# Kernel tuning notes

Hardware: AMD Instinct MI355X
Metric: run time of the kernel (lower is better)

## Reference

```python
import jax, jax.numpy as jnp
import numpy as np

NEG_INF = -9e15  # matches the torch -9000000000000000.0 mask value
LRELU_SLOPE = 0.01  # torch nn.LeakyReLU default


def setup_inputs() -> dict:
    key = jax.random.key(0)
    k1, k2, k3, k4 = jax.random.split(key, 4)
    N, F_in, F_out = 8192, 256, 128
    x = jax.random.normal(k1, (N, F_in), dtype=jnp.float32)
    adj = jax.random.randint(k2, (N, N), 0, 2, dtype=jnp.int32)
    # xavier_uniform with gain=1.414
    limW = 1.414 * np.sqrt(6.0 / (F_in + F_out))
    W = jax.random.uniform(k3, (F_in, F_out), minval=-limW, maxval=limW, dtype=jnp.float32)
    lima = 1.414 * np.sqrt(6.0 / (2 * F_out + 1))
    a = jax.random.uniform(k4, (2 * F_out, 1), minval=-lima, maxval=lima, dtype=jnp.float32)
    return {"x": x, "adj": adj, "W": W, "a": a}


def reference(x, adj, W, a):
    # h: [N, F_out]
    h = x @ W
    F_out = h.shape[1]
    a1 = a[:F_out, 0]   # attention vector for source node i
    a2 = a[F_out:, 0]   # attention vector for target node j
    # e[i, j] = leaky_relu(h_i . a1 + h_j . a2) -- equivalent to the repeat/cat
    # construction without materializing the [N, N, 2F] tensor.
    e = (h @ a1)[:, None] + (h @ a2)[None, :]  # [N, N]
    e = jnp.where(e > 0, e, LRELU_SLOPE * e)
    scores = jnp.where(adj > 0, e, NEG_INF)
    attention = jax.nn.softmax(scores, axis=1)  # dropout omitted (eval mode)
    h_prime = attention @ h  # [N, F_out]
    return jax.nn.elu(h_prime)
```

## Files before the change

### kernel.cpp

```cpp
#include <hip/hip_runtime.h>
#include <hip/hip_bf16.h>
#include <stdint.h>


#define N_NODES 8192
#define F_INF   256
#define F_OUT   128
#define LRELU   0.01f

typedef __bf16 bf16x8 __attribute__((ext_vector_type(8)));
typedef float  f32x4  __attribute__((ext_vector_type(4)));
using bf16 = __hip_bfloat16;

__device__ __forceinline__ float b2f(bf16 v) { return __bfloat162float(v); }
__device__ __forceinline__ bf16  f2b(float v) { return __float2bfloat16(v); }

__global__ __launch_bounds__(256) void k_xw(const float* __restrict__ x,
                                            const float* __restrict__ W,
                                            const float* __restrict__ a,
                                            bf16* __restrict__ hT,
                                            float* __restrict__ s1,
                                            float* __restrict__ s2) {
    __shared__ __align__(16) bf16 WTh[F_OUT][F_INF + 8];
    __shared__ __align__(16) bf16 WTl[F_OUT][F_INF + 8];
    __shared__ __align__(16) bf16 XSh[32][72];
    __shared__ __align__(16) bf16 XSl[32][72];
    __shared__ float a1s[F_OUT], a2s[F_OUT], s1L[32], s2L[32];
    const int tid  = threadIdx.x;
    const int lane = tid & 63, wave = tid >> 6;
    const int i0   = blockIdx.x * 32;
    if (tid < F_OUT) { a1s[tid] = a[tid]; a2s[tid] = a[tid + F_OUT]; }
    if (tid < 32)    { s1L[tid] = 0.f; s2L[tid] = 0.f; }
    for (int idx = tid; idx < (F_INF * F_OUT) / 8; idx += 256) {
        int k  = idx >> 4;
        int n0 = (idx & 15) * 8;
        const float* src = W + (size_t)k * F_OUT + n0;
        float4 va = *(const float4*)(src);
        float4 vb = *(const float4*)(src + 4);
        float v[8] = {va.x, va.y, va.z, va.w, vb.x, vb.y, vb.z, vb.w};
#pragma unroll
        for (int c = 0; c < 8; ++c) {
            bf16 hi = f2b(v[c]);
            WTh[n0 + c][k] = hi;
            WTl[n0 + c][k] = f2b(v[c] - b2f(hi));
        }
    }
    __syncthreads();
    f32x4 acc[4];
#pragma unroll
    for (int t = 0; t < 4; ++t) acc[t] = {0.f, 0.f, 0.f, 0.f};
    const int m = lane & 15, quad = lane >> 4;
    const int rt = wave & 1, cH = wave >> 1;
    for (int kc = 0; kc < F_INF / 64; ++kc) {
        const int k0 = kc * 64;
        {
            int part = tid & 7;
            int r    = tid >> 3;
            const float* src = x + (size_t)(i0 + r) * F_INF + k0 + part * 8;
            float4 va = *(const float4*)(src);
            float4 vb = *(const float4*)(src + 4);
            float v[8] = {va.x, va.y, va.z, va.w, vb.x, vb.y, vb.z, vb.w};
            __align__(16) bf16 th[8];
            __align__(16) bf16 tl[8];
#pragma unroll
            for (int c = 0; c < 8; ++c) {
                bf16 hi = f2b(v[c]);
                th[c] = hi;
                tl[c] = f2b(v[c] - b2f(hi));
            }
            *(uint4*)(&XSh[r][part * 8]) = *(const uint4*)th;
            *(uint4*)(&XSl[r][part * 8]) = *(const uint4*)tl;
        }
        __syncthreads();
#pragma unroll
        for (int ks = 0; ks < 2; ++ks) {
            bf16x8 ah = *(const bf16x8*)(&XSh[rt * 16 + m][ks * 32 + quad * 8]);
            bf16x8 al = *(const bf16x8*)(&XSl[rt * 16 + m][ks * 32 + quad * 8]);
#pragma unroll
            for (int c = 0; c < 4; ++c) {
                const int ct = cH * 4 + c;
                bf16x8 bh = *(const bf16x8*)(&WTh[ct * 16 + m][k0 + ks * 32 + quad * 8]);
                bf16x8 bl = *(const bf16x8*)(&WTl[ct * 16 + m][k0 + ks * 32 + quad * 8]);
                acc[c] = __builtin_amdgcn_mfma_f32_16x16x32_bf16(al, bh, acc[c], 0, 0, 0);
                acc[c] = __builtin_amdgcn_mfma_f32_16x16x32_bf16(ah, bl, acc[c], 0, 0, 0);
                acc[c] = __builtin_amdgcn_mfma_f32_16x16x32_bf16(ah, bh, acc[c], 0, 0, 0);
            }
        }
        __syncthreads();
    }
    float p1[4] = {0.f, 0.f, 0.f, 0.f}, p2[4] = {0.f, 0.f, 0.f, 0.f};
#pragma unroll
    for (int c = 0; c < 4; ++c) {
        const int f = (cH * 4 + c) * 16 + m;
        const float w1 = a1s[f], w2 = a2s[f];
#pragma unroll
        for (int r = 0; r < 4; ++r) { p1[r] += acc[c][r] * w1; p2[r] += acc[c][r] * w2; }
    }
#pragma unroll
    for (int r = 0; r < 4; ++r) {
        const int row = rt * 16 + quad * 4 + r;
        atomicAdd(&s1L[row], p1[r]);
        atomicAdd(&s2L[row], p2[r]);
    }
#pragma unroll
    for (int c = 0; c < 4; ++c) {
        const int f = (cH * 4 + c) * 16 + m;
#pragma unroll
        for (int r = 0; r < 4; ++r) {
            const int i = i0 + rt * 16 + quad * 4 + r;
            hT[(size_t)f * N_NODES + i] = f2b(acc[c][r]);
        }
    }
    __syncthreads();
    if (tid < 32) { s1[i0 + tid] = s1L[tid]; s2[i0 + tid] = s2L[tid]; }
}

__global__ __launch_bounds__(256) void k_max(const float* __restrict__ s2,
                                             float* __restrict__ mg) {
    __shared__ float red[256];
    int tid = threadIdx.x;
    float m = -1e30f;
    for (int j = tid; j < N_NODES; j += 256) m = fmaxf(m, s2[j]);
    red[tid] = m;
    __syncthreads();
    for (int s = 128; s > 0; s >>= 1) {
        if (tid < s) red[tid] = fmaxf(red[tid], red[tid + s]);
        __syncthreads();
    }
    if (tid == 0) mg[0] = red[0];
}

__global__ __launch_bounds__(256) void k_attn(const int* __restrict__ adj,
                                              const float* __restrict__ s1g,
                                              const float* __restrict__ s2g,
                                              const float* __restrict__ mg,
                                              const bf16* __restrict__ hT,
                                              float* __restrict__ Of,
                                              float* __restrict__ lp) {
    __shared__ __align__(16) bf16 HS[F_OUT][72];
    __shared__ __align__(16) bf16 PS[32][72];
    __shared__ float s1s[32], mis[32], lsum[32];
    const int tid  = threadIdx.x;
    const int lane = tid & 63, wave = tid >> 6;
    const int i0    = blockIdx.x * 32;
    const int jq    = blockIdx.y;
    const int jbase = jq * (N_NODES / 4);
    if (tid < 32) {
        float s1v = s1g[i0 + tid];
        float t   = s1v + mg[0];
        s1s[tid]  = s1v;
        mis[tid]  = t > 0.f ? t : LRELU * t;
        lsum[tid] = 0.f;
    }
    __syncthreads();
    const int jpart = tid & 15;
    const int rA    = tid >> 4;
    float lacc0 = 0.f, lacc1 = 0.f;
    const int m = lane & 15, quad = lane >> 4;
    const int cg = wave;
    f32x4 acc[2][2];
#pragma unroll
    for (int rt = 0; rt < 2; ++rt)
#pragma unroll
        for (int c = 0; c < 2; ++c) acc[rt][c] = {0.f, 0.f, 0.f, 0.f};

    for (int jc = 0; jc < (N_NODES / 4) / 64; ++jc) {
        const int j0 = jbase + jc * 64;
        {
            int part = tid & 7, fr = tid >> 3;
#pragma unroll
            for (int p = 0; p < 4; ++p) {
                int f   = fr + p * 32;
                uint4 v = *(const uint4*)(hT + (size_t)f * N_NODES + j0 + part * 8);
                *(uint4*)(&HS[f][part * 8]) = v;
            }
        }
        {
            float4 s2v = *(const float4*)(s2g + j0 + jpart * 4);
#pragma unroll
            for (int p = 0; p < 2; ++p) {
                int r = rA + p * 16;
                const int4 av = *(const int4*)(adj + (size_t)(i0 + r) * N_NODES + j0 + jpart * 4);
                const float s1v = s1s[r], miv = mis[r];
                float t;
                t = s1v + s2v.x; t = t > 0.f ? t : LRELU * t;
                bf16 b0 = f2b((av.x > 0) ? __expf(t - miv) : 0.f);
                t = s1v + s2v.y; t = t > 0.f ? t : LRELU * t;
                bf16 b1 = f2b((av.y > 0) ? __expf(t - miv) : 0.f);
                t = s1v + s2v.z; t = t > 0.f ? t : LRELU * t;
                bf16 b2 = f2b((av.z > 0) ? __expf(t - miv) : 0.f);
                t = s1v + s2v.w; t = t > 0.f ? t : LRELU * t;
                bf16 b3 = f2b((av.w > 0) ? __expf(t - miv) : 0.f);
                float wsum = (b2f(b0) + b2f(b1)) + (b2f(b2) + b2f(b3));
                if (p == 0) lacc0 += wsum; else lacc1 += wsum;
                PS[r][jpart * 4 + 0] = b0;
                PS[r][jpart * 4 + 1] = b1;
                PS[r][jpart * 4 + 2] = b2;
                PS[r][jpart * 4 + 3] = b3;
            }
        }
        __syncthreads();
#pragma unroll
        for (int ks = 0; ks < 2; ++ks) {
#pragma unroll
            for (int rt = 0; rt < 2; ++rt) {
                bf16x8 af = *(const bf16x8*)(&PS[rt * 16 + m][ks * 32 + quad * 8]);
#pragma unroll
                for (int c = 0; c < 2; ++c) {
                    bf16x8 bfr = *(const bf16x8*)(&HS[(cg * 2 + c) * 16 + m][ks * 32 + quad * 8]);
                    acc[rt][c] = __builtin_amdgcn_mfma_f32_16x16x32_bf16(af, bfr, acc[rt][c], 0, 0, 0);
                }
            }
        }
        __syncthreads();
    }
    atomicAdd(&lsum[rA], lacc0);
    atomicAdd(&lsum[rA + 16], lacc1);
    __syncthreads();
    if (tid < 32) lp[(size_t)jq * N_NODES + i0 + tid] = lsum[tid];
#pragma unroll
    for (int rt = 0; rt < 2; ++rt) {
#pragma unroll
        for (int c = 0; c < 2; ++c) {
            const int f = (cg * 2 + c) * 16 + m;
#pragma unroll
            for (int r = 0; r < 4; ++r) {
                const int i = i0 + rt * 16 + quad * 4 + r;
                Of[((size_t)jq * N_NODES + i) * F_OUT + f] = acc[rt][c][r];
            }
        }
    }
}

__global__ __launch_bounds__(256) void k_comb(const float* __restrict__ Of,
                                              const float* __restrict__ lp,
                                              float* __restrict__ out) {
    size_t gid = (size_t)blockIdx.x * 256 + threadIdx.x;
    int i = (int)(gid >> 7);
    float s = 0.f, l = 0.f;
#pragma unroll
    for (int q = 0; q < 4; ++q) {
        s += Of[(size_t)q * (N_NODES * (size_t)F_OUT) + gid];
        l += lp[q * N_NODES + i];
    }
    float o = s / l;
    out[gid] = o > 0.f ? o : __expf(o) - 1.f;
}

extern "C" void kernel_launch(void* const* d_in, const int* in_sizes, int n_in,
                              void* d_out, int out_size, void* d_ws, size_t ws_size,
                              hipStream_t stream) {
    (void)out_size; (void)ws_size;
    const float* x   = nullptr;
    const int*   adj = nullptr;
    const float* W   = nullptr;
    const float* a   = nullptr;
    for (int ii = 0; ii < n_in; ++ii) {
        int sz = in_sizes[ii];
        if      (sz == N_NODES * F_INF)  x   = (const float*)d_in[ii];
        else if (sz == F_INF * F_OUT)    W   = (const float*)d_in[ii];
        else if (sz == 2 * F_OUT)        a   = (const float*)d_in[ii];
        else                             adj = (const int*)d_in[ii];
    }
    float* out = (float*)d_out;

    char* ws = (char*)d_ws;
    bf16*  hT = (bf16*)ws;  ws += (size_t)F_OUT * N_NODES * 2;
    float* s1 = (float*)ws; ws += N_NODES * 4;
    float* s2 = (float*)ws; ws += N_NODES * 4;
    float* mg = (float*)ws; ws += 256;
    float* lp = (float*)ws; ws += 4 * N_NODES * 4;
    float* Of = (float*)ws;

    k_xw  <<<N_NODES / 32, 256, 0, stream>>>(x, W, a, hT, s1, s2);
    k_max <<<1, 256, 0, stream>>>(s2, mg);
    k_attn<<<dim3(N_NODES / 32, 4), 256, 0, stream>>>(adj, s1, s2, mg, hT, Of, lp);
    k_comb<<<(N_NODES * F_OUT) / 256, 256, 0, stream>>>(Of, lp, out);
}
```

Baseline: 441.1 us.

## Compute attention weights in registers as MFMA A-fragments and prefetch next tiles

```diff
diff --git a/kernel.cpp b/kernel.cpp
--- a/kernel.cpp
+++ b/kernel.cpp
@@ -130,105 +130,109 @@
     if (tid == 0) mg[0] = red[0];
 }
 
-__global__ __launch_bounds__(256) void k_attn(const int* __restrict__ adj,
-                                              const float* __restrict__ s1g,
-                                              const float* __restrict__ s2g,
-                                              const float* __restrict__ mg,
-                                              const bf16* __restrict__ hT,
-                                              float* __restrict__ Of,
-                                              float* __restrict__ lp) {
+__global__ __launch_bounds__(256, 4) void k_attn(const int* __restrict__ adj,
+                                                 const float* __restrict__ s1g,
+                                                 const float* __restrict__ s2g,
+                                                 const float* __restrict__ mg,
+                                                 const bf16* __restrict__ hT,
+                                                 float* __restrict__ Of,
+                                                 float* __restrict__ lp) {
     __shared__ __align__(16) bf16 HS[F_OUT][72];
-    __shared__ __align__(16) bf16 PS[32][72];
-    __shared__ float s1s[32], mis[32], lsum[32];
+    __shared__ float s2s[2048];
+    __shared__ float lsum[32];
     const int tid  = threadIdx.x;
     const int lane = tid & 63, wave = tid >> 6;
+    const int m = lane & 15, quad = lane >> 4;
+    const int rt = wave & 1, kh = wave >> 1;
     const int i0    = blockIdx.x * 32;
     const int jq    = blockIdx.y;
-    const int jbase = jq * (N_NODES / 4);
-    if (tid < 32) {
-        float s1v = s1g[i0 + tid];
-        float t   = s1v + mg[0];
-        s1s[tid]  = s1v;
-        mis[tid]  = t > 0.f ? t : LRELU * t;
-        lsum[tid] = 0.f;
-    }
-    __syncthreads();
-    const int jpart = tid & 15;
-    const int rA    = tid >> 4;
-    float lacc0 = 0.f, lacc1 = 0.f;
-    const int m = lane & 15, quad = lane >> 4;
-    const int cg = wave;
-    f32x4 acc[2][2];
-#pragma unroll
-    for (int rt = 0; rt < 2; ++rt)
-#pragma unroll
-        for (int c = 0; c < 2; ++c) acc[rt][c] = {0.f, 0.f, 0.f, 0.f};
-
-    for (int jc = 0; jc < (N_NODES / 4) / 64; ++jc) {
-        const int j0 = jbase + jc * 64;
-        {
-            int part = tid & 7, fr = tid >> 3;
-#pragma unroll
-            for (int p = 0; p < 4; ++p) {
-                int f   = fr + p * 32;
-                uint4 v = *(const uint4*)(hT + (size_t)f * N_NODES + j0 + part * 8);
-                *(uint4*)(&HS[f][part * 8]) = v;
+    const int jbase = jq * 2048;
+    const int irow  = i0 + rt * 16 + m;
+    const float s1v = s1g[irow];
+    const float tmi = s1v + mg[0];
+    const float mi  = fmaxf(tmi, LRELU * tmi);
+    if (tid < 32) lsum[tid] = 0.f;
+    for (int c = tid; c < 2048 / 4; c += 256)
+        *(float4*)&s2s[c * 4] = *(const float4*)(s2g + jbase + c * 4);
+    const int part = tid & 7, fr = tid >> 3;
+    const bf16* hTp = hT + jbase + part * 8;
+    {
+        uint4 v0 = *(const uint4*)(hTp + (size_t)(fr +  0) * N_NODES);
+        uint4 v1 = *(const uint4*)(hTp + (size_t)(fr + 32) * N_NODES);
+        uint4 v2 = *(const uint4*)(hTp + (size_t)(fr + 64) * N_NODES);
+        uint4 v3 = *(const uint4*)(hTp + (size_t)(fr + 96) * N_NODES);
+        *(uint4*)&HS[fr +  0][part * 8] = v0;
+        *(uint4*)&HS[fr + 32][part * 8] = v1;
+        *(uint4*)&HS[fr + 64][part * 8] = v2;
+        *(uint4*)&HS[fr + 96][part * 8] = v3;
+    }
+    const int jloc = kh * 32 + quad * 8;
+    const int4* arowp = (const int4*)(adj + (size_t)irow * N_NODES + jbase);
+    int4 av0 = arowp[0 * 16 + jloc / 4];
+    int4 av1 = arowp[0 * 16 + jloc / 4 + 1];
+    float lacc = 0.f;
+    f32x4 acc[8];
+#pragma unroll
+    for (int c = 0; c < 8; ++c) acc[c] = {0.f, 0.f, 0.f, 0.f};
+    __syncthreads();
+
+    for (int jc = 0; jc < 32; ++jc) {
+        const int jn = (jc < 31) ? jc + 1 : 31;
+        uint4 h0 = *(const uint4*)(hTp + (size_t)(fr +  0) * N_NODES + jn * 64);
+        uint4 h1 = *(const uint4*)(hTp + (size_t)(fr + 32) * N_NODES + jn * 64);
+        uint4 h2 = *(const uint4*)(hTp + (size_t)(fr + 64) * N_NODES + jn * 64);
+        uint4 h3 = *(const uint4*)(hTp + (size_t)(fr + 96) * N_NODES + jn * 64);
+        const int am[8] = {av0.x, av0.y, av0.z, av0.w, av1.x, av1.y, av1.z, av1.w};
+        const float* s2p = &s2s[jc * 64 + jloc];
+        __align__(16) bf16 a8[8];
+#pragma unroll
+        for (int t = 0; t < 8; ++t) {
+            float e = s1v + s2p[t];
+            e = fmaxf(e, LRELU * e);
+            float w = (am[t] > 0) ? __expf(e - mi) : 0.f;
+            bf16 b = f2b(w);
+            a8[t] = b;
+            lacc += b2f(b);
+        }
+        bf16x8 afrag = *(const bf16x8*)a8;
+        av0 = arowp[jn * 16 + jloc / 4];
+        av1 = arowp[jn * 16 + jloc / 4 + 1];
+#pragma unroll
+        for (int c = 0; c < 8; ++c) {
+            bf16x8 bfr = *(const bf16x8*)(&HS[c * 16 + m][jloc]);
+            acc[c] = __builtin_amdgcn_mfma_f32_16x16x32_bf16(afrag, bfr, acc[c], 0, 0, 0);
+        }
+        __syncthreads();
+        *(uint4*)&HS[fr +  0][part * 8] = h0;
+        *(uint4*)&HS[fr + 32][part * 8] = h1;
+        *(uint4*)&HS[fr + 64][part * 8] = h2;
+        *(uint4*)&HS[fr + 96][part * 8] = h3;
+        __syncthreads();
+    }
+    lacc += __shfl_xor(lacc, 16);
+    lacc += __shfl_xor(lacc, 32);
+    if (quad == 0) atomicAdd(&lsum[rt * 16 + m], lacc);
+    __syncthreads();
+    if (tid < 32) lp[(size_t)jq * N_NODES + i0 + tid] = lsum[tid];
+    float* scr = (float*)&HS[0][0];
+    if (kh == 1) {
+#pragma unroll
+        for (int c = 0; c < 8; ++c)
+#pragma unroll
+            for (int r = 0; r < 4; ++r)
+                scr[(rt * 16 + quad * 4 + r) * 128 + c * 16 + m] = acc[c][r];
+    }
+    __syncthreads();
+    if (kh == 0) {
+#pragma unroll
+        for (int c = 0; c < 8; ++c)
+#pragma unroll
+            for (int r = 0; r < 4; ++r) {
+                const int row = rt * 16 + quad * 4 + r;
+                const int f   = c * 16 + m;
+                Of[((size_t)jq * N_NODES + i0 + row) * F_OUT + f] =
+                    acc[c][r] + scr[row * 128 + f];
             }
-        }
-        {
-            float4 s2v = *(const float4*)(s2g + j0 + jpart * 4);
-#pragma unroll
-            for (int p = 0; p < 2; ++p) {
-                int r = rA + p * 16;
-                const int4 av = *(const int4*)(adj + (size_t)(i0 + r) * N_NODES + j0 + jpart * 4);
-                const float s1v = s1s[r], miv = mis[r];
-                float t;
-                t = s1v + s2v.x; t = t > 0.f ? t : LRELU * t;
-                bf16 b0 = f2b((av.x > 0) ? __expf(t - miv) : 0.f);
-                t = s1v + s2v.y; t = t > 0.f ? t : LRELU * t;
-                bf16 b1 = f2b((av.y > 0) ? __expf(t - miv) : 0.f);
-                t = s1v + s2v.z; t = t > 0.f ? t : LRELU * t;
-                bf16 b2 = f2b((av.z > 0) ? __expf(t - miv) : 0.f);
-                t = s1v + s2v.w; t = t > 0.f ? t : LRELU * t;
-                bf16 b3 = f2b((av.w > 0) ? __expf(t - miv) : 0.f);
-                float wsum = (b2f(b0) + b2f(b1)) + (b2f(b2) + b2f(b3));
-                if (p == 0) lacc0 += wsum; else lacc1 += wsum;
-                PS[r][jpart * 4 + 0] = b0;
-                PS[r][jpart * 4 + 1] = b1;
-                PS[r][jpart * 4 + 2] = b2;
-                PS[r][jpart * 4 + 3] = b3;
-            }
-        }
-        __syncthreads();
-#pragma unroll
-        for (int ks = 0; ks < 2; ++ks) {
-#pragma unroll
-            for (int rt = 0; rt < 2; ++rt) {
-                bf16x8 af = *(const bf16x8*)(&PS[rt * 16 + m][ks * 32 + quad * 8]);
-#pragma unroll
-                for (int c = 0; c < 2; ++c) {
-                    bf16x8 bfr = *(const bf16x8*)(&HS[(cg * 2 + c) * 16 + m][ks * 32 + quad * 8]);
-                    acc[rt][c] = __builtin_amdgcn_mfma_f32_16x16x32_bf16(af, bfr, acc[rt][c], 0, 0, 0);
-                }
-            }
-        }
-        __syncthreads();
-    }
-    atomicAdd(&lsum[rA], lacc0);
-    atomicAdd(&lsum[rA + 16], lacc1);
-    __syncthreads();
-    if (tid < 32) lp[(size_t)jq * N_NODES + i0 + tid] = lsum[tid];
-#pragma unroll
-    for (int rt = 0; rt < 2; ++rt) {
-#pragma unroll
-        for (int c = 0; c < 2; ++c) {
-            const int f = (cg * 2 + c) * 16 + m;
-#pragma unroll
-            for (int r = 0; r < 4; ++r) {
-                const int i = i0 + rt * 16 + quad * 4 + r;
-                Of[((size_t)jq * N_NODES + i) * F_OUT + f] = acc[rt][c][r];
-            }
-        }
     }
 }
 
```

After: 437.0 us. Within noise of the previous version (-0.9%).
